# Kernel optimization log

Measured on AMD Instinct MI355X. Metric: run time of the kernel, lower is better.

The kernel has to match this reference:

```python
import jax, jax.numpy as jnp
import numpy as np

B, S, H, NH, D = 2, 2048, 2048, 16, 128
SCALE = D ** -0.5


def _rotate_half(x):
    x1, x2 = jnp.split(x, 2, axis=-1)
    return jnp.concatenate([-x2, x1], axis=-1)


def setup_inputs() -> dict:
    key = jax.random.key(0)
    ks = jax.random.split(key, 6)
    hidden_states = jax.random.normal(ks[0], (B, S, H), dtype=jnp.float32)
    # causal additive mask (batch, 1, q_len, kv_len)
    causal = jnp.where(jnp.tril(jnp.ones((S, S), dtype=bool)), 0.0, -1e9).astype(jnp.float32)
    attention_mask = jnp.broadcast_to(causal[None, None], (B, 1, S, S))
    # standard RoPE tables, theta=10000
    inv_freq = 1.0 / (10000.0 ** (jnp.arange(0, D, 2, dtype=jnp.float32) / D))
    t = jnp.arange(S, dtype=jnp.float32)
    freqs = jnp.einsum('s,f->sf', t, inv_freq)
    emb = jnp.concatenate([freqs, freqs], axis=-1)  # (S, D)
    rope_cos = jnp.cos(emb)[None, None]  # (1,1,S,D)
    rope_sin = jnp.sin(emb)[None, None]
    w_std = H ** -0.5
    Wq = jax.random.normal(ks[1], (H, NH * D), dtype=jnp.float32) * w_std
    Wk = jax.random.normal(ks[2], (H, D), dtype=jnp.float32) * w_std
    Wv = jax.random.normal(ks[3], (H, D), dtype=jnp.float32) * w_std
    Wo = jax.random.normal(ks[4], (NH * D, H), dtype=jnp.float32) * ((NH * D) ** -0.5)
    return {
        'hidden_states': hidden_states,
        'attention_mask': attention_mask,
        'rope_cos': rope_cos,
        'rope_sin': rope_sin,
        'Wq': Wq, 'Wk': Wk, 'Wv': Wv, 'Wo': Wo,
    }


def reference(hidden_states, attention_mask, rope_cos, rope_sin, Wq, Wk, Wv, Wo):
    b, s, _ = hidden_states.shape
    q = (hidden_states @ Wq).reshape(b, s, NH, D).transpose(0, 2, 1, 3)  # (b,h,s,d)
    k = (hidden_states @ Wk)[:, None]  # (b,1,s,d) single shared KV head
    v = (hidden_states @ Wv)[:, None]
    # inline RoPE on q and the shared k
    q = q * rope_cos + _rotate_half(q) * rope_sin
    k = k * rope_cos + _rotate_half(k) * rope_sin
    k = k[:, 0]  # (b,s,d); broadcast over heads instead of expand
    v = v[:, 0]
    scores = jnp.einsum('bhqd,bkd->bhqk', q, k) * SCALE + attention_mask
    attn = jax.nn.softmax(scores.astype(jnp.float32), axis=-1).astype(q.dtype)
    out = jnp.einsum('bhqk,bkd->bhqd', attn, v)
    out = out.transpose(0, 2, 1, 3).reshape(b, s, NH * D)
    return out @ Wo
```

## Files before the change

### kernel.cpp

```cpp
#include <hip/hip_runtime.h>
#include <hip/hip_bf16.h>

#define NB 2
#define NS 2048
#define NHID 2048
#define NHEAD 16
#define ND 128
#define NM (NB*NS)

typedef __attribute__((ext_vector_type(8))) short s16x8;
typedef __attribute__((ext_vector_type(4))) float f32x4;

__device__ __forceinline__ short f2bf(float x) {
  unsigned u = __float_as_uint(x);
  u = (u + 0x7fffu + ((u >> 16) & 1u)) >> 16;
  return (short)u;
}

__device__ __forceinline__ int colmap(int wc, int ni) {
  return (ni < 2) ? (wc*32 + ni*16) : (64 + wc*32 + (ni-2)*16);
}

__device__ __forceinline__ void gload16(const short* g, short* l) {
  __builtin_amdgcn_global_load_lds(
      (const __attribute__((address_space(1))) void*)g,
      (__attribute__((address_space(3))) void*)l, 16, 0, 0);
}

__global__ __launch_bounds__(256) void cvt_f32_bf16(const float* __restrict__ src,
                                                    short* __restrict__ dst, int n4) {
  int i = blockIdx.x*256 + threadIdx.x;
  if (i >= n4) return;
  const float4 v = reinterpret_cast<const float4*>(src)[i];
  unsigned long long pk =
      (unsigned long long)(unsigned short)f2bf(v.x)
    | ((unsigned long long)(unsigned short)f2bf(v.y) << 16)
    | ((unsigned long long)(unsigned short)f2bf(v.z) << 32)
    | ((unsigned long long)(unsigned short)f2bf(v.w) << 48);
  reinterpret_cast<unsigned long long*>(dst)[i] = pk;
}

__global__ __launch_bounds__(256) void cvtT(const float* __restrict__ src,
                                            short* __restrict__ dst, int K, int N) {
  __shared__ float t[32][33];
  const int n0 = blockIdx.x*32, k0 = blockIdx.y*32;
  const int tx = threadIdx.x & 31, ty = threadIdx.x >> 5;
  #pragma unroll
  for (int i = 0; i < 4; ++i)
    t[ty + 8*i][tx] = src[(size_t)(k0 + ty + 8*i)*N + n0 + tx];
  __syncthreads();
  #pragma unroll
  for (int i = 0; i < 4; ++i)
    dst[(size_t)(n0 + ty + 8*i)*K + k0 + tx] = f2bf(t[tx][ty + 8*i]);
}

__global__ __launch_bounds__(256) void gemm_qkv(
    const short* __restrict__ hsb, const short* __restrict__ WqT,
    const short* __restrict__ WkT, const short* __restrict__ WvT,
    const float* __restrict__ ropeC, const float* __restrict__ ropeS,
    short* __restrict__ Qb, short* __restrict__ Kb, short* __restrict__ Vb)
{
  const int tid = threadIdx.x;
  const int lane = tid & 63, wid = tid >> 6;
  const int wr = wid >> 1, wc = wid & 1;
  const int l15 = lane & 15, l4 = lane >> 4;
  const int m0 = blockIdx.x * 128;
  const int ny = blockIdx.y;
  const short* Bt = (ny < 16) ? (WqT + (size_t)ny*128*2048) : (ny == 16 ? WkT : WvT);

  __shared__ short Al[128][32];
  __shared__ short Bl[128][32];

  f32x4 acc[4][4];
  const f32x4 zf = {0.f,0.f,0.f,0.f};
  #pragma unroll
  for (int i=0;i<4;++i)
    #pragma unroll
    for (int j=0;j<4;++j) acc[i][j] = zf;

  const int srow = tid >> 2;
  const int scol = (tid & 3) * 8;
  const short* Ap0 = hsb + (size_t)(m0 + srow)*2048 + scol;
  const short* Ap1 = hsb + (size_t)(m0 + 64 + srow)*2048 + scol;
  const short* Bp0 = Bt + (size_t)srow*2048 + scol;
  const short* Bp1 = Bt + (size_t)(64 + srow)*2048 + scol;
  short* AL0 = &Al[0][0] + tid*8;
  short* AL1 = &Al[0][0] + 2048 + tid*8;
  short* BL0 = &Bl[0][0] + tid*8;
  short* BL1 = &Bl[0][0] + 2048 + tid*8;

  for (int kt = 0; kt < 64; ++kt) {
    const int k0 = kt * 32;
    __syncthreads();
    gload16(Ap0 + k0, AL0);
    gload16(Ap1 + k0, AL1);
    gload16(Bp0 + k0, BL0);
    gload16(Bp1 + k0, BL1);
    __syncthreads();
    s16x8 af[4], bfr[4];
    #pragma unroll
    for (int mi=0; mi<4; ++mi) af[mi] = *(const s16x8*)&Al[wr*64 + mi*16 + l15][l4*8];
    #pragma unroll
    for (int ni=0; ni<4; ++ni) bfr[ni] = *(const s16x8*)&Bl[colmap(wc,ni) + l15][l4*8];
    #pragma unroll
    for (int mi=0; mi<4; ++mi)
      #pragma unroll
      for (int ni=0; ni<4; ++ni)
        acc[mi][ni] = __builtin_amdgcn_mfma_f32_16x16x32_bf16(af[mi], bfr[ni], acc[mi][ni], 0,0,0);
  }

  const bool isQ = (ny < 16), isK = (ny == 16);
  #pragma unroll
  for (int mi=0; mi<4; ++mi) {
    #pragma unroll
    for (int r=0; r<4; ++r) {
      const int mrow = m0 + wr*64 + mi*16 + l4*4 + r;
      const int s = mrow & 2047;
      const int bb = mrow >> 11;
      if (!isQ && !isK) {
        #pragma unroll
        for (int ni=0; ni<4; ++ni) {
          const int d = colmap(wc,ni) + l15;
          Vb[(size_t)mrow*128 + d] = f2bf(acc[mi][ni][r]);
        }
      } else {
        #pragma unroll
        for (int ni=0; ni<2; ++ni) {
          const int d = colmap(wc,ni) + l15;
          const float c0 = ropeC[s*128 + d],      s0 = ropeS[s*128 + d];
          const float c1 = ropeC[s*128 + d + 64], s1 = ropeS[s*128 + d + 64];
          const float x0 = acc[mi][ni][r], x1 = acc[mi][ni+2][r];
          const float y0 = x0*c0 - x1*s0;
          const float y1 = x1*c1 + x0*s1;
          if (isK) {
            Kb[(size_t)mrow*128 + d]      = f2bf(y0);
            Kb[(size_t)mrow*128 + d + 64] = f2bf(y1);
          } else {
            const size_t base = ((size_t)(bb*16 + ny)*2048 + s)*128;
            Qb[base + d]      = f2bf(y0);
            Qb[base + d + 64] = f2bf(y1);
          }
        }
      }
    }
  }
}

__device__ __forceinline__ void attn_tile_proc(
    const s16x8 (&qf)[4], int qtile, int t, int wid, int l15, int l4,
    short (&Kl)[64][136], short (&Vt)[128][72], short (&Pl)[4][16][72],
    f32x4 (&o)[8], float (&m_run)[4], float (&l_run)[4])
{
  const float CEXP = 0.08838834764831845f * 1.44269504088896340f;
  const f32x4 zf = {0.f,0.f,0.f,0.f};
  f32x4 sc[4];
  #pragma unroll
  for (int n=0;n<4;++n) sc[n] = zf;
  #pragma unroll
  for (int kk=0; kk<4; ++kk) {
    #pragma unroll
    for (int n=0; n<4; ++n) {
      s16x8 kf = *(const s16x8*)&Kl[n*16 + l15][kk*32 + l4*8];
      sc[n] = __builtin_amdgcn_mfma_f32_16x16x32_bf16(qf[kk], kf, sc[n], 0,0,0);
    }
  }

  float p[4][4];
  const bool diag = (t == qtile);
  #pragma unroll
  for (int n=0;n<4;++n)
    #pragma unroll
    for (int r=0;r<4;++r) {
      float sv = sc[n][r];
      if (diag) {
        const int qg  = wid*16 + l4*4 + r;
        const int kvg = n*16 + l15;
        if (kvg > qg) sv = -1e30f;
      }
      p[n][r] = sv;
    }
  float pm[4];
  #pragma unroll
  for (int r=0;r<4;++r)
    pm[r] = fmaxf(fmaxf(p[0][r], p[1][r]), fmaxf(p[2][r], p[3][r]));
  #pragma unroll
  for (int d=1; d<16; d<<=1)
    #pragma unroll
    for (int r=0;r<4;++r) pm[r] = fmaxf(pm[r], __shfl_xor(pm[r], d));
  float alpha[4];
  #pragma unroll
  for (int r=0;r<4;++r) {
    const float mn = fmaxf(m_run[r], pm[r]);
    alpha[r] = exp2f((m_run[r] - mn) * CEXP);
    m_run[r] = mn;
  }
  #pragma unroll
  for (int n=0;n<4;++n)
    #pragma unroll
    for (int r=0;r<4;++r)
      p[n][r] = exp2f((p[n][r] - m_run[r]) * CEXP);
  float rs[4];
  #pragma unroll
  for (int r=0;r<4;++r) rs[r] = (p[0][r]+p[1][r])+(p[2][r]+p[3][r]);
  #pragma unroll
  for (int d=1; d<16; d<<=1)
    #pragma unroll
    for (int r=0;r<4;++r) rs[r] += __shfl_xor(rs[r], d);
  #pragma unroll
  for (int r=0;r<4;++r) l_run[r] = l_run[r]*alpha[r] + rs[r];
  #pragma unroll
  for (int i=0;i<8;++i)
    #pragma unroll
    for (int r=0;r<4;++r) o[i][r] *= alpha[r];

  #pragma unroll
  for (int n=0;n<4;++n)
    #pragma unroll
    for (int r=0;r<4;++r)
      Pl[wid][l4*4 + r][n*16 + l15] = f2bf(p[n][r]);

  s16x8 pa[2];
  #pragma unroll
  for (int kb=0; kb<2; ++kb) pa[kb] = *(const s16x8*)&Pl[wid][l15][kb*32 + l4*8];
  #pragma unroll
  for (int kb=0; kb<2; ++kb)
    #pragma unroll
    for (int d8=0; d8<8; ++d8) {
      s16x8 vf = *(const s16x8*)&Vt[d8*16 + l15][kb*32 + l4*8];
      o[d8] = __builtin_amdgcn_mfma_f32_16x16x32_bf16(pa[kb], vf, o[d8], 0,0,0);
    }
}

__global__ __launch_bounds__(256) void attn_fwd(
    const short* __restrict__ Qb, const short* __restrict__ Kb,
    const short* __restrict__ Vb, short* __restrict__ Ob)
{
  const int tid = threadIdx.x;
  const int lane = tid & 63, wid = tid >> 6;
  const int l15 = lane & 15, l4 = lane >> 4;
  const int pr = blockIdx.x, h = blockIdx.y, b = blockIdx.z;
  const int lo = pr, hi = 31 - pr;

  __shared__ short Kl[64][136];
  __shared__ short Vt[128][72];
  __shared__ short Pl[4][16][72];

  s16x8 qfL[4], qfH[4];
  {
    const short* QpL = Qb + ((size_t)(b*16 + h)*2048 + lo*64 + wid*16 + l15)*128 + l4*8;
    const short* QpH = Qb + ((size_t)(b*16 + h)*2048 + hi*64 + wid*16 + l15)*128 + l4*8;
    #pragma unroll
    for (int kk=0; kk<4; ++kk) { qfL[kk] = *(const s16x8*)(QpL + kk*32);
                                 qfH[kk] = *(const s16x8*)(QpH + kk*32); }
  }

  float mL[4], lL[4], mH[4], lH[4];
  f32x4 oL[8], oH[8];
  const f32x4 zf = {0.f,0.f,0.f,0.f};
  #pragma unroll
  for (int r=0;r<4;++r){ mL[r]=-1e30f; lL[r]=0.f; mH[r]=-1e30f; lH[r]=0.f; }
  #pragma unroll
  for (int i=0;i<8;++i){ oL[i]=zf; oH[i]=zf; }

  for (int t=0; t<=hi; ++t) {
    const int kv0 = t*64;
    __syncthreads();
    #pragma unroll
    for (int rep=0; rep<4; ++rep) {
      const int c = tid + rep*256;
      {
        const int row = c >> 4, off = (c & 15) * 8;
        *(uint4*)&Kl[row][off] = *(const uint4*)(Kb + ((size_t)(b*2048 + kv0 + row))*128 + off);
      }
      {
        const int row = c & 63, off = (c >> 6) * 8;
        uint4 vv = *(const uint4*)(Vb + ((size_t)(b*2048 + kv0 + row))*128 + off);
        const short* vs = (const short*)&vv;
        #pragma unroll
        for (int j=0;j<8;++j) Vt[off + j][row] = vs[j];
      }
    }
    __syncthreads();

    attn_tile_proc(qfH, hi, t, wid, l15, l4, Kl, Vt, Pl, oH, mH, lH);
    if (t <= lo)
      attn_tile_proc(qfL, lo, t, wid, l15, l4, Kl, Vt, Pl, oL, mL, lL);
  }

  #pragma unroll
  for (int r=0;r<4;++r) {
    const float invL = 1.0f / lL[r];
    const float invH = 1.0f / lH[r];
    const size_t baseL = ((size_t)(b*2048) + lo*64 + wid*16 + l4*4 + r)*2048 + (size_t)h*128;
    const size_t baseH = ((size_t)(b*2048) + hi*64 + wid*16 + l4*4 + r)*2048 + (size_t)h*128;
    #pragma unroll
    for (int d8=0; d8<8; ++d8) {
      Ob[baseL + d8*16 + l15] = f2bf(oL[d8][r] * invL);
      Ob[baseH + d8*16 + l15] = f2bf(oH[d8][r] * invH);
    }
  }
}

__global__ __launch_bounds__(256) void gemm_out(
    const short* __restrict__ Ob, const short* __restrict__ WoT,
    float* __restrict__ out)
{
  const int tid = threadIdx.x;
  const int lane = tid & 63, wid = tid >> 6;
  const int wr = wid >> 1, wc = wid & 1;
  const int l15 = lane & 15, l4 = lane >> 4;
  const int m0 = blockIdx.x * 128;
  const int n0 = blockIdx.y * 128;

  __shared__ short Al[128][32];
  __shared__ short Bl[128][32];

  f32x4 acc[4][4];
  const f32x4 zf = {0.f,0.f,0.f,0.f};
  #pragma unroll
  for (int i=0;i<4;++i)
    #pragma unroll
    for (int j=0;j<4;++j) acc[i][j] = zf;

  const int srow = tid >> 2;
  const int scol = (tid & 3) * 8;
  const short* Ap0 = Ob + (size_t)(m0 + srow)*2048 + scol;
  const short* Ap1 = Ob + (size_t)(m0 + 64 + srow)*2048 + scol;
  const short* Bp0 = WoT + (size_t)(n0 + srow)*2048 + scol;
  const short* Bp1 = WoT + (size_t)(n0 + 64 + srow)*2048 + scol;
  short* AL0 = &Al[0][0] + tid*8;
  short* AL1 = &Al[0][0] + 2048 + tid*8;
  short* BL0 = &Bl[0][0] + tid*8;
  short* BL1 = &Bl[0][0] + 2048 + tid*8;

  for (int kt = 0; kt < 64; ++kt) {
    const int k0 = kt * 32;
    __syncthreads();
    gload16(Ap0 + k0, AL0);
    gload16(Ap1 + k0, AL1);
    gload16(Bp0 + k0, BL0);
    gload16(Bp1 + k0, BL1);
    __syncthreads();
    s16x8 af[4], bfr[4];
    #pragma unroll
    for (int mi=0; mi<4; ++mi) af[mi] = *(const s16x8*)&Al[wr*64 + mi*16 + l15][l4*8];
    #pragma unroll
    for (int ni=0; ni<4; ++ni) bfr[ni] = *(const s16x8*)&Bl[colmap(wc,ni) + l15][l4*8];
    #pragma unroll
    for (int mi=0; mi<4; ++mi)
      #pragma unroll
      for (int ni=0; ni<4; ++ni)
        acc[mi][ni] = __builtin_amdgcn_mfma_f32_16x16x32_bf16(af[mi], bfr[ni], acc[mi][ni], 0,0,0);
  }

  #pragma unroll
  for (int mi=0; mi<4; ++mi)
    #pragma unroll
    for (int r=0; r<4; ++r) {
      const int mrow = m0 + wr*64 + mi*16 + l4*4 + r;
      #pragma unroll
      for (int ni=0; ni<4; ++ni)
        out[(size_t)mrow*2048 + n0 + colmap(wc,ni) + l15] = acc[mi][ni][r];
    }
}

extern "C" void kernel_launch(void* const* d_in, const int* in_sizes, int n_in,
                              void* d_out, int out_size, void* d_ws, size_t ws_size,
                              hipStream_t stream) {
  const float* hidden = (const float*)d_in[0];
  const float* ropeC  = (const float*)d_in[2];
  const float* ropeS  = (const float*)d_in[3];
  const float* Wq     = (const float*)d_in[4];
  const float* Wk     = (const float*)d_in[5];
  const float* Wv     = (const float*)d_in[6];
  const float* Wo     = (const float*)d_in[7];
  float* out = (float*)d_out;
  char* ws = (char*)d_ws;

  short* hsb = (short*)(ws + 0);
  short* WqT = (short*)(ws + 16777216);
  short* WkT = (short*)(ws + 25165824);
  short* WvT = (short*)(ws + 25690112);
  short* WoT = (short*)(ws + 26214400);
  short* Qb  = (short*)(ws + 34603008);
  short* Kb  = (short*)(ws + 51380224);
  short* Vb  = (short*)(ws + 52428800);
  short* Ob  = hsb;

  cvt_f32_bf16<<<dim3((NM*NHID/4 + 255)/256), dim3(256), 0, stream>>>(hidden, hsb, NM*NHID/4);
  cvtT<<<dim3(64,64), dim3(256), 0, stream>>>(Wq, WqT, 2048, 2048);
  cvtT<<<dim3(4, 64), dim3(256), 0, stream>>>(Wk, WkT, 2048, 128);
  cvtT<<<dim3(4, 64), dim3(256), 0, stream>>>(Wv, WvT, 2048, 128);
  cvtT<<<dim3(64,64), dim3(256), 0, stream>>>(Wo, WoT, 2048, 2048);

  gemm_qkv<<<dim3(NM/128, 18), dim3(256), 0, stream>>>(hsb, WqT, WkT, WvT, ropeC, ropeS, Qb, Kb, Vb);
  attn_fwd<<<dim3(16, NHEAD, NB), dim3(256), 0, stream>>>(Qb, Kb, Vb, Ob);
  gemm_out<<<dim3(NM/128, 2048/128), dim3(256), 0, stream>>>(Ob, WoT, out);
}
```

Baseline: 461.8 us.

## Read K and pre-transposed V directly from global memory in attention

Adds a kernel that transposes V into a d-major layout once, then has the attention kernel load MFMA K and V fragments straight from global memory instead of staging them through LDS. This removes both per-tile __syncthreads and the scalar transposed LDS stores for V. The grid is flattened to 1D with a swizzle so that blocks sharing a batch and head land on the same XCD, improving L2 reuse of the shared K/V. The trade-offs are an extra transpose launch and strided, less coalesced global loads for the fragments, which now rely on cache hits.

Result: slower. 511.4 us (+10.7%).

```diff
diff --git a/kernel.cpp b/kernel.cpp
--- a/kernel.cpp
+++ b/kernel.cpp
@@ -52,6 +52,21 @@
   #pragma unroll
   for (int i = 0; i < 4; ++i)
     dst[(size_t)(n0 + ty + 8*i)*K + k0 + tx] = f2bf(t[tx][ty + 8*i]);
+}
+
+__global__ __launch_bounds__(256) void trans_v(const short* __restrict__ src,
+                                               short* __restrict__ dst) {
+  __shared__ short t[32][40];
+  const int c0 = blockIdx.x*32;
+  const int r0 = blockIdx.y*32;
+  const int tx = threadIdx.x & 31, ty = threadIdx.x >> 5;
+  #pragma unroll
+  for (int i = 0; i < 4; ++i)
+    t[ty + 8*i][tx] = src[(size_t)(r0 + ty + 8*i)*128 + c0 + tx];
+  __syncthreads();
+  #pragma unroll
+  for (int i = 0; i < 4; ++i)
+    dst[(size_t)(c0 + ty + 8*i)*4096 + r0 + tx] = t[tx][ty + 8*i];
 }
 
 __global__ __launch_bounds__(256) void gemm_qkv(
@@ -148,7 +163,8 @@
 
 __device__ __forceinline__ void attn_tile_proc(
     const s16x8 (&qf)[4], int qtile, int t, int wid, int l15, int l4,
-    short (&Kl)[64][136], short (&Vt)[128][72], short (&Pl)[4][16][72],
+    const short* __restrict__ Ktile, const short* __restrict__ Vtile,
+    short (&Plw)[16][72],
     f32x4 (&o)[8], float (&m_run)[4], float (&l_run)[4])
 {
   const float CEXP = 0.08838834764831845f * 1.44269504088896340f;
@@ -157,13 +173,12 @@
   #pragma unroll
   for (int n=0;n<4;++n) sc[n] = zf;
   #pragma unroll
-  for (int kk=0; kk<4; ++kk) {
+  for (int kk=0; kk<4; ++kk)
     #pragma unroll
     for (int n=0; n<4; ++n) {
-      s16x8 kf = *(const s16x8*)&Kl[n*16 + l15][kk*32 + l4*8];
+      s16x8 kf = *(const s16x8*)(Ktile + (size_t)(n*16 + l15)*128 + kk*32 + l4*8);
       sc[n] = __builtin_amdgcn_mfma_f32_16x16x32_bf16(qf[kk], kf, sc[n], 0,0,0);
     }
-  }
 
   float p[4][4];
   const bool diag = (t == qtile);
@@ -217,32 +232,32 @@
   for (int n=0;n<4;++n)
     #pragma unroll
     for (int r=0;r<4;++r)
-      Pl[wid][l4*4 + r][n*16 + l15] = f2bf(p[n][r]);
+      Plw[l4*4 + r][n*16 + l15] = f2bf(p[n][r]);
 
   s16x8 pa[2];
   #pragma unroll
-  for (int kb=0; kb<2; ++kb) pa[kb] = *(const s16x8*)&Pl[wid][l15][kb*32 + l4*8];
+  for (int kb=0; kb<2; ++kb) pa[kb] = *(const s16x8*)&Plw[l15][kb*32 + l4*8];
   #pragma unroll
   for (int kb=0; kb<2; ++kb)
     #pragma unroll
     for (int d8=0; d8<8; ++d8) {
-      s16x8 vf = *(const s16x8*)&Vt[d8*16 + l15][kb*32 + l4*8];
+      s16x8 vf = *(const s16x8*)(Vtile + (size_t)(d8*16 + l15)*4096 + kb*32 + l4*8);
       o[d8] = __builtin_amdgcn_mfma_f32_16x16x32_bf16(pa[kb], vf, o[d8], 0,0,0);
     }
 }
 
 __global__ __launch_bounds__(256) void attn_fwd(
     const short* __restrict__ Qb, const short* __restrict__ Kb,
-    const short* __restrict__ Vb, short* __restrict__ Ob)
+    const short* __restrict__ VbT, short* __restrict__ Ob)
 {
   const int tid = threadIdx.x;
   const int lane = tid & 63, wid = tid >> 6;
   const int l15 = lane & 15, l4 = lane >> 4;
-  const int pr = blockIdx.x, h = blockIdx.y, b = blockIdx.z;
+  const int bid = blockIdx.x;
+  const int wg = (bid & 7)*64 + (bid >> 3);
+  const int pr = wg & 15, h = (wg >> 4) & 15, b = wg >> 8;
   const int lo = pr, hi = 31 - pr;
 
-  __shared__ short Kl[64][136];
-  __shared__ short Vt[128][72];
   __shared__ short Pl[4][16][72];
 
   s16x8 qfL[4], qfH[4];
@@ -263,28 +278,11 @@
   for (int i=0;i<8;++i){ oL[i]=zf; oH[i]=zf; }
 
   for (int t=0; t<=hi; ++t) {
-    const int kv0 = t*64;
-    __syncthreads();
-    #pragma unroll
-    for (int rep=0; rep<4; ++rep) {
-      const int c = tid + rep*256;
-      {
-        const int row = c >> 4, off = (c & 15) * 8;
-        *(uint4*)&Kl[row][off] = *(const uint4*)(Kb + ((size_t)(b*2048 + kv0 + row))*128 + off);
-      }
-      {
-        const int row = c & 63, off = (c >> 6) * 8;
-        uint4 vv = *(const uint4*)(Vb + ((size_t)(b*2048 + kv0 + row))*128 + off);
-        const short* vs = (const short*)&vv;
-        #pragma unroll
-        for (int j=0;j<8;++j) Vt[off + j][row] = vs[j];
-      }
-    }
-    __syncthreads();
-
-    attn_tile_proc(qfH, hi, t, wid, l15, l4, Kl, Vt, Pl, oH, mH, lH);
+    const short* Ktile = Kb + ((size_t)b*2048 + t*64)*128;
+    const short* Vtile = VbT + (size_t)b*2048 + t*64;
+    attn_tile_proc(qfH, hi, t, wid, l15, l4, Ktile, Vtile, Pl[wid], oH, mH, lH);
     if (t <= lo)
-      attn_tile_proc(qfL, lo, t, wid, l15, l4, Kl, Vt, Pl, oL, mL, lL);
+      attn_tile_proc(qfL, lo, t, wid, l15, l4, Ktile, Vtile, Pl[wid], oL, mL, lL);
   }
 
   #pragma unroll
@@ -385,6 +383,7 @@
   short* Qb  = (short*)(ws + 34603008);
   short* Kb  = (short*)(ws + 51380224);
   short* Vb  = (short*)(ws + 52428800);
+  short* VbT = (short*)(ws + 53477376);
   short* Ob  = hsb;
 
   cvt_f32_bf16<<<dim3((NM*NHID/4 + 255)/256), dim3(256), 0, stream>>>(hidden, hsb, NM*NHID/4);
@@ -394,6 +393,7 @@
   cvtT<<<dim3(64,64), dim3(256), 0, stream>>>(Wo, WoT, 2048, 2048);
 
   gemm_qkv<<<dim3(NM/128, 18), dim3(256), 0, stream>>>(hsb, WqT, WkT, WvT, ropeC, ropeS, Qb, Kb, Vb);
-  attn_fwd<<<dim3(16, NHEAD, NB), dim3(256), 0, stream>>>(Qb, Kb, Vb, Ob);
+  trans_v<<<dim3(4, 128), dim3(256), 0, stream>>>(Vb, VbT);
+  attn_fwd<<<dim3(512), dim3(256), 0, stream>>>(Qb, Kb, VbT, Ob);
   gemm_out<<<dim3(NM/128, 2048/128), dim3(256), 0, stream>>>(Ob, WoT, out);
 }
```
